# Optimization experiments

Measured on AMD Instinct MI355X. Metric: run time of the kernel, lower is better.

The kernel has to match this reference:

```python
import jax, jax.numpy as jnp
import numpy as np

HC = 4           # hc_mult
ITERS = 20       # hc_sinkhorn_iters
EPS = 1e-6       # hc_eps
NORM_EPS = 1e-6  # rms_norm_eps


def setup_inputs() -> dict:
    key = jax.random.key(0)
    k = jax.random.split(key, 4)
    B, S, H = 1, 4096, 4096
    mix = (2 + HC) * HC  # 24
    hidden_states = jax.random.normal(k[0], (B, S, HC, H), jnp.float32)
    hc_fn = jax.random.normal(k[1], (mix, HC * H), jnp.float32) * 0.02
    hc_base = jax.random.normal(k[2], (mix,), jnp.float32) * 0.02
    hc_scale = jnp.ones((3,), jnp.float32)
    norm_weight = jnp.ones((H,), jnp.float32)
    w_inner = jax.random.normal(k[3], (H, H), jnp.float32) * 0.02
    return {
        "hidden_states": hidden_states,
        "hc_fn": hc_fn,
        "hc_base": hc_base,
        "hc_scale": hc_scale,
        "norm_weight": norm_weight,
        "w_inner": w_inner,
    }


def reference(hidden_states, hc_fn, hc_base, hc_scale, norm_weight, w_inner):
    B, S, hc, H = hidden_states.shape
    # RMS stat over the flattened (hc*H) feature dim
    flat = hidden_states.reshape(B, S, hc * H).astype(jnp.float32)
    rs = jax.lax.rsqrt(jnp.mean(jnp.square(flat), axis=-1, keepdims=True) + NORM_EPS)
    mixes = jnp.einsum('bsd,md->bsm', flat, hc_fn) * rs  # [B,S,(2+hc)*hc]

    ps, qs, cs = hc_scale[0], hc_scale[1], hc_scale[2]
    pre = jax.nn.sigmoid(mixes[..., :hc] * ps + hc_base[:hc]) + EPS           # [B,S,hc]
    post = jax.nn.sigmoid(mixes[..., hc:2 * hc] * qs + hc_base[hc:2 * hc]) + EPS
    comb = jax.nn.sigmoid(
        mixes[..., 2 * hc:].reshape(B, S, hc, hc) * cs
        + hc_base[2 * hc:].reshape(hc, hc)
    ) + EPS  # [B,S,hc,hc]

    # 20-iter Sinkhorn row/column normalization
    def sink(_, c):
        c = c / (jnp.sum(c, axis=-1, keepdims=True) + EPS)
        return c / (jnp.sum(c, axis=-2, keepdims=True) + EPS)
    comb = jax.lax.fori_loop(0, ITERS, sink, comb)

    # weighted stream reduction -> [B,S,H]
    reduced = jnp.einsum('bsh,bshd->bsd', pre, hidden_states)

    # norm + inner sub-block (RMSNorm then dense projection)
    nr = jax.lax.rsqrt(jnp.mean(jnp.square(reduced), axis=-1, keepdims=True) + NORM_EPS)
    normed = reduced * nr * norm_weight
    out = jnp.einsum('bsd,ed->bse', normed, w_inner)  # [B,S,H]

    # broadcast back to streams: post-gated write + Sinkhorn-mixed residual
    expanded = post[..., None] * out[:, :, None, :] \
        + jnp.einsum('bshk,bskd->bshd', comb, hidden_states)
    return expanded.astype(hidden_states.dtype)
```

## Files before the change

### kernel.cpp

```cpp
#include <hip/hip_runtime.h>
#include <math.h>

#define S_DIM 4096
#define H_DIM 4096
#define HC_N 4
#define HD_DIM 16384
#define MIXN 24
#define SINK_IT 20
#define KSPL 32

typedef float f32x4 __attribute__((ext_vector_type(4)));
typedef __bf16 bf16x8 __attribute__((ext_vector_type(8)));
typedef unsigned short u16x8 __attribute__((ext_vector_type(8)));
typedef unsigned short u16x4 __attribute__((ext_vector_type(4)));

__device__ __forceinline__ unsigned short f2bf(float f) {
  unsigned u = __builtin_bit_cast(unsigned, f);
  u += 0x7FFFu + ((u >> 16) & 1u);
  return (unsigned short)(u >> 16);
}
__device__ __forceinline__ float bf2f(unsigned short h) {
  return __builtin_bit_cast(float, (unsigned)h << 16);
}

__global__ __launch_bounds__(256) void k_w2bf(const float* __restrict__ w,
                                              unsigned short* __restrict__ wb,
                                              const float* __restrict__ fn,
                                              unsigned short* __restrict__ fnb) {
  const int b = blockIdx.x;
  if (b < 8192) {
    const size_t i = (size_t)b * 2048 + threadIdx.x * 8;
    f32x4 a = *(const f32x4*)(w + i);
    f32x4 c = *(const f32x4*)(w + i + 4);
    u16x8 o;
    o[0] = f2bf(a.x); o[1] = f2bf(a.y); o[2] = f2bf(a.z); o[3] = f2bf(a.w);
    o[4] = f2bf(c.x); o[5] = f2bf(c.y); o[6] = f2bf(c.z); o[7] = f2bf(c.w);
    *(u16x8*)(wb + i) = o;
  } else if (b < 8384) {
    const size_t i = (size_t)(b - 8192) * 2048 + threadIdx.x * 8;
    f32x4 a = *(const f32x4*)(fn + i);
    f32x4 c = *(const f32x4*)(fn + i + 4);
    u16x8 o;
    o[0] = f2bf(a.x); o[1] = f2bf(a.y); o[2] = f2bf(a.z); o[3] = f2bf(a.w);
    o[4] = f2bf(c.x); o[5] = f2bf(c.y); o[6] = f2bf(c.z); o[7] = f2bf(c.w);
    *(u16x8*)(fnb + i) = o;
  } else {
    const size_t i = 393216 + (size_t)(b - 8384) * 2048 + threadIdx.x * 8;
    u16x8 o = {0, 0, 0, 0, 0, 0, 0, 0};
    *(u16x8*)(fnb + i) = o;
  }
}

__global__ __launch_bounds__(256) void k_mixgemm(const float* __restrict__ hs,
                                                 const unsigned short* __restrict__ fnb,
                                                 float* __restrict__ mixpart,
                                                 float* __restrict__ sumsqpart) {
  const int rt = blockIdx.x;
  const int p = blockIdx.y;
  const int tid = threadIdx.x, lane = tid & 63, wave = tid >> 6;
  const int r16 = lane & 15, kq = lane >> 4;
  const int row0 = rt * 128 + wave * 32;
  const size_t kbase = (size_t)p * 512 + kq * 8;

  f32x4 acc[2][2];
  f32x4 zero = {0.f, 0.f, 0.f, 0.f};
  acc[0][0] = zero; acc[0][1] = zero; acc[1][0] = zero; acc[1][1] = zero;
  float ss0 = 0.f, ss1 = 0.f;

  const float* a0 = hs + (size_t)(row0 + r16) * HD_DIM + kbase;
  const float* a1 = hs + (size_t)(row0 + 16 + r16) * HD_DIM + kbase;
  const unsigned short* b0p = fnb + (size_t)r16 * HD_DIM + kbase;
  const unsigned short* b1p = fnb + (size_t)(16 + r16) * HD_DIM + kbase;

#pragma unroll 4
  for (int kk = 0; kk < 512; kk += 32) {
    const f32x4 va0 = *(const f32x4*)(a0 + kk);
    const f32x4 va0b = *(const f32x4*)(a0 + kk + 4);
    const f32x4 va1 = *(const f32x4*)(a1 + kk);
    const f32x4 va1b = *(const f32x4*)(a1 + kk + 4);
    const bf16x8 fb0 = *(const bf16x8*)(b0p + kk);
    const bf16x8 fb1 = *(const bf16x8*)(b1p + kk);
    ss0 += va0.x * va0.x + va0.y * va0.y + va0.z * va0.z + va0.w * va0.w
         + va0b.x * va0b.x + va0b.y * va0b.y + va0b.z * va0b.z + va0b.w * va0b.w;
    ss1 += va1.x * va1.x + va1.y * va1.y + va1.z * va1.z + va1.w * va1.w
         + va1b.x * va1b.x + va1b.y * va1b.y + va1b.z * va1b.z + va1b.w * va1b.w;
    bf16x8 fa0, fa1;
    fa0[0] = (__bf16)va0.x; fa0[1] = (__bf16)va0.y; fa0[2] = (__bf16)va0.z; fa0[3] = (__bf16)va0.w;
    fa0[4] = (__bf16)va0b.x; fa0[5] = (__bf16)va0b.y; fa0[6] = (__bf16)va0b.z; fa0[7] = (__bf16)va0b.w;
    fa1[0] = (__bf16)va1.x; fa1[1] = (__bf16)va1.y; fa1[2] = (__bf16)va1.z; fa1[3] = (__bf16)va1.w;
    fa1[4] = (__bf16)va1b.x; fa1[5] = (__bf16)va1b.y; fa1[6] = (__bf16)va1b.z; fa1[7] = (__bf16)va1b.w;
    acc[0][0] = __builtin_amdgcn_mfma_f32_16x16x32_bf16(fa0, fb0, acc[0][0], 0, 0, 0);
    acc[0][1] = __builtin_amdgcn_mfma_f32_16x16x32_bf16(fa0, fb1, acc[0][1], 0, 0, 0);
    acc[1][0] = __builtin_amdgcn_mfma_f32_16x16x32_bf16(fa1, fb0, acc[1][0], 0, 0, 0);
    acc[1][1] = __builtin_amdgcn_mfma_f32_16x16x32_bf16(fa1, fb1, acc[1][1], 0, 0, 0);
  }

  ss0 += __shfl_xor(ss0, 16, 64); ss0 += __shfl_xor(ss0, 32, 64);
  ss1 += __shfl_xor(ss1, 16, 64); ss1 += __shfl_xor(ss1, 32, 64);
  if (lane < 16) {
    sumsqpart[(size_t)(row0 + lane) * KSPL + p] = ss0;
    sumsqpart[(size_t)(row0 + 16 + lane) * KSPL + p] = ss1;
  }

  const int cr = (lane >> 4) * 4, cc = lane & 15;
#pragma unroll
  for (int mi = 0; mi < 2; mi++)
#pragma unroll
    for (int ni = 0; ni < 2; ni++) {
      const int col = ni * 16 + cc;
      if (col < MIXN) {
#pragma unroll
        for (int j = 0; j < 4; j++) {
          const int row = row0 + mi * 16 + cr + j;
          mixpart[((size_t)row * KSPL + p) * MIXN + col] = acc[mi][ni][j];
        }
      }
    }
}

__global__ __launch_bounds__(256) void k_gates(const float* __restrict__ mixpart,
                                               const float* __restrict__ sumsqpart,
                                               const float* __restrict__ hbase,
                                               const float* __restrict__ hscale,
                                               float* __restrict__ gates) {
  const int row = blockIdx.x * 256 + threadIdx.x;
  float sumsq = 0.f;
  const float* sp = sumsqpart + (size_t)row * KSPL;
#pragma unroll
  for (int p = 0; p < KSPL; p++) sumsq += sp[p];
  float mr[MIXN];
#pragma unroll
  for (int m = 0; m < MIXN; m++) mr[m] = 0.f;
  const float* mp = mixpart + (size_t)row * KSPL * MIXN;
  for (int p = 0; p < KSPL; p++) {
#pragma unroll
    for (int m = 0; m < MIXN; m++) mr[m] += mp[p * MIXN + m];
  }
  const float rs = rsqrtf(sumsq * (1.0f / HD_DIM) + 1e-6f);
  const float ps = hscale[0], qs = hscale[1], cs = hscale[2];
  float g[MIXN];
#pragma unroll
  for (int m = 0; m < MIXN; m++) {
    const float sc = (m < 4) ? ps : ((m < 8) ? qs : cs);
    const float x = mr[m] * rs * sc + hbase[m];
    g[m] = 1.0f / (1.0f + expf(-x)) + 1e-6f;
  }
  for (int t = 0; t < SINK_IT; t++) {
#pragma unroll
    for (int i = 0; i < 4; i++) {
      const float s = g[8 + i * 4 + 0] + g[8 + i * 4 + 1] + g[8 + i * 4 + 2] + g[8 + i * 4 + 3] + 1e-6f;
#pragma unroll
      for (int j = 0; j < 4; j++) g[8 + i * 4 + j] /= s;
    }
#pragma unroll
    for (int j = 0; j < 4; j++) {
      const float s = g[8 + 0 + j] + g[8 + 4 + j] + g[8 + 8 + j] + g[8 + 12 + j] + 1e-6f;
#pragma unroll
      for (int i = 0; i < 4; i++) g[8 + i * 4 + j] /= s;
    }
  }
  float* go = gates + (size_t)row * MIXN;
#pragma unroll
  for (int m = 0; m < MIXN; m++) go[m] = g[m];
}

__global__ __launch_bounds__(256) void k_reduce_norm(const float* __restrict__ hs,
                                                     const float* __restrict__ gates,
                                                     const float* __restrict__ nw,
                                                     unsigned short* __restrict__ normed) {
  const int s = blockIdx.x, tid = threadIdx.x;
  const int lane = tid & 63, wave = tid >> 6;
  const float* g = gates + (size_t)s * MIXN;
  const float p0 = g[0], p1 = g[1], p2 = g[2], p3 = g[3];
  const size_t base = (size_t)s * HC_N * H_DIM;

  f32x4 red[4];
  float ssq = 0.f;
#pragma unroll
  for (int it = 0; it < 4; ++it) {
    const int d4 = it * 256 + tid;
    f32x4 a = *(const f32x4*)(hs + base + (size_t)0 * H_DIM + (size_t)d4 * 4);
    f32x4 b = *(const f32x4*)(hs + base + (size_t)1 * H_DIM + (size_t)d4 * 4);
    f32x4 c = *(const f32x4*)(hs + base + (size_t)2 * H_DIM + (size_t)d4 * 4);
    f32x4 d = *(const f32x4*)(hs + base + (size_t)3 * H_DIM + (size_t)d4 * 4);
    f32x4 v = p0 * a + p1 * b + p2 * c + p3 * d;
    red[it] = v;
    ssq += v.x * v.x + v.y * v.y + v.z * v.z + v.w * v.w;
  }
#pragma unroll
  for (int off = 32; off >= 1; off >>= 1) ssq += __shfl_xor(ssq, off, 64);
  __shared__ float ls[4];
  if (lane == 0) ls[wave] = ssq;
  __syncthreads();
  const float tot = ls[0] + ls[1] + ls[2] + ls[3];
  const float nr = rsqrtf(tot * (1.0f / H_DIM) + 1e-6f);
#pragma unroll
  for (int it = 0; it < 4; ++it) {
    const int d4 = it * 256 + tid;
    f32x4 w = *(const f32x4*)(nw + (size_t)d4 * 4);
    f32x4 v = red[it] * nr;
    v = v * w;
    u16x4 o;
    o[0] = f2bf(v.x); o[1] = f2bf(v.y); o[2] = f2bf(v.z); o[3] = f2bf(v.w);
    *(u16x4*)(normed + (size_t)s * H_DIM + (size_t)d4 * 4) = o;
  }
}

__device__ __forceinline__ void gload_lds16(const unsigned short* g, unsigned short* l) {
  __builtin_amdgcn_global_load_lds(
      (const __attribute__((address_space(1))) unsigned int*)(const void*)g,
      (__attribute__((address_space(3))) unsigned int*)(void*)l, 16, 0, 0);
}

__global__ __launch_bounds__(256, 4) void k_gemm(const unsigned short* __restrict__ A,
                                                 const unsigned short* __restrict__ B,
                                                 unsigned short* __restrict__ C) {
  __shared__ __align__(16) unsigned short sA[128 * 32];
  __shared__ __align__(16) unsigned short sB[128 * 32];
  const int tid = threadIdx.x;
  const int lane = tid & 63, wave = tid >> 6;
  const int bm = blockIdx.y, bn = blockIdx.x;
  const int wm = wave >> 1, wn = wave & 1;

  f32x4 zero = {0.f, 0.f, 0.f, 0.f};
  f32x4 acc[4][4];
#pragma unroll
  for (int mi = 0; mi < 4; mi++)
#pragma unroll
    for (int ni = 0; ni < 4; ni++) acc[mi][ni] = zero;

  const int strow = lane >> 2;
  const int stk = (((lane & 3) ^ ((lane >> 3) & 3)) * 8);
  const unsigned short* ga = A + (size_t)(bm * 128) * 4096;
  const unsigned short* gb = B + (size_t)(bn * 128) * 4096;
  const int c0 = wave * 2, c1 = wave * 2 + 1;

  const int rb = lane & 15;
  const int fk = (((lane >> 4) ^ ((lane >> 1) & 3)) * 8);

  for (int kk = 0; kk < 4096; kk += 32) {
    gload_lds16(ga + (size_t)(c0 * 16 + strow) * 4096 + kk + stk, sA + c0 * 512);
    gload_lds16(ga + (size_t)(c1 * 16 + strow) * 4096 + kk + stk, sA + c1 * 512);
    gload_lds16(gb + (size_t)(c0 * 16 + strow) * 4096 + kk + stk, sB + c0 * 512);
    gload_lds16(gb + (size_t)(c1 * 16 + strow) * 4096 + kk + stk, sB + c1 * 512);
    __syncthreads();

    bf16x8 af[4], bfr[4];
#pragma unroll
    for (int mi = 0; mi < 4; mi++)
      af[mi] = *(const bf16x8*)(sA + (wm * 64 + mi * 16 + rb) * 32 + fk);
#pragma unroll
    for (int ni = 0; ni < 4; ni++)
      bfr[ni] = *(const bf16x8*)(sB + (wn * 64 + ni * 16 + rb) * 32 + fk);
#pragma unroll
    for (int mi = 0; mi < 4; mi++)
#pragma unroll
      for (int ni = 0; ni < 4; ni++)
        acc[mi][ni] = __builtin_amdgcn_mfma_f32_16x16x32_bf16(af[mi], bfr[ni], acc[mi][ni], 0, 0, 0);
    __syncthreads();
  }

  const int cr = (lane >> 4) * 4, cc = lane & 15;
#pragma unroll
  for (int mi = 0; mi < 4; mi++)
#pragma unroll
    for (int ni = 0; ni < 4; ni++)
#pragma unroll
      for (int j = 0; j < 4; j++) {
        const int row = bm * 128 + wm * 64 + mi * 16 + cr + j;
        const int col = bn * 128 + wn * 64 + ni * 16 + cc;
        C[(size_t)row * 4096 + col] = f2bf(acc[mi][ni][j]);
      }
}

__global__ __launch_bounds__(256) void k_expand(const float* __restrict__ hs,
                                                const unsigned short* __restrict__ outb,
                                                const float* __restrict__ gates,
                                                float* __restrict__ y) {
  const int s = blockIdx.x, tid = threadIdx.x;
  const float* g = gates + (size_t)s * MIXN;
  float post[4], cb[4][4];
#pragma unroll
  for (int h = 0; h < 4; h++) post[h] = g[4 + h];
#pragma unroll
  for (int h = 0; h < 4; h++)
#pragma unroll
    for (int k = 0; k < 4; k++) cb[h][k] = g[8 + h * 4 + k];

  const size_t base = (size_t)s * HC_N * H_DIM;
#pragma unroll
  for (int it = 0; it < 4; ++it) {
    const int d4 = it * 256 + tid;
    f32x4 hv[4];
#pragma unroll
    for (int k = 0; k < 4; k++)
      hv[k] = *(const f32x4*)(hs + base + (size_t)k * H_DIM + (size_t)d4 * 4);
    u16x4 ob = *(const u16x4*)(outb + (size_t)s * H_DIM + (size_t)d4 * 4);
    f32x4 o = {bf2f(ob[0]), bf2f(ob[1]), bf2f(ob[2]), bf2f(ob[3])};
#pragma unroll
    for (int h = 0; h < 4; h++) {
      f32x4 e = post[h] * o + cb[h][0] * hv[0] + cb[h][1] * hv[1] + cb[h][2] * hv[2] + cb[h][3] * hv[3];
      *(f32x4*)(y + base + (size_t)h * H_DIM + (size_t)d4 * 4) = e;
    }
  }
}

extern "C" void kernel_launch(void* const* d_in, const int* in_sizes, int n_in,
                              void* d_out, int out_size, void* d_ws, size_t ws_size,
                              hipStream_t stream) {
  const float* hs = (const float*)d_in[0];
  const float* fn = (const float*)d_in[1];
  const float* hbase = (const float*)d_in[2];
  const float* hscale = (const float*)d_in[3];
  const float* nw = (const float*)d_in[4];
  const float* wi = (const float*)d_in[5];
  float* y = (float*)d_out;

  char* ws = (char*)d_ws;
  float* gates = (float*)(ws);
  float* sumsqpart = (float*)(ws + 524288);
  float* mixpart = (float*)(ws + 1048576);
  unsigned short* fnb = (unsigned short*)(ws + 13631488);
  unsigned short* normed = (unsigned short*)(ws + 16777216);
  unsigned short* wb = (unsigned short*)(ws + 50331648);
  unsigned short* outb = (unsigned short*)(ws + 83886080);

  k_w2bf<<<8448, 256, 0, stream>>>(wi, wb, fn, fnb);
  k_mixgemm<<<dim3(32, 32), 256, 0, stream>>>(hs, fnb, mixpart, sumsqpart);
  k_gates<<<16, 256, 0, stream>>>(mixpart, sumsqpart, hbase, hscale, gates);
  k_reduce_norm<<<4096, 256, 0, stream>>>(hs, gates, nw, normed);
  k_gemm<<<dim3(32, 32), 256, 0, stream>>>(normed, wb, outb);
  k_expand<<<4096, 256, 0, stream>>>(hs, outb, gates, y);
}
```

Baseline: 434.9 us.

## Emit bf16 hidden-state copy in mix GEMM and reuse it downstream

The mix GEMM already converts hidden_states to bf16, so it now also writes that bf16 copy to workspace. The reduce/norm and expand kernels then read this half-size copy instead of the fp32 tensor, cutting the bytes of the two later full passes. The split-K factor is doubled and the partial buffers are transposed. The gates kernel now spreads the partial-sum reduction across four wave groups through shared memory. The trade-off is an extra 128MB write, a large workspace requirement (with an fp32 fallback when it is too small), and a bf16-rounded residual term in the output.

After: 440.4 us. About the same (+1.3%).

```diff
diff --git a/kernel.cpp b/kernel.cpp
--- a/kernel.cpp
+++ b/kernel.cpp
@@ -7,7 +7,7 @@
 #define HD_DIM 16384
 #define MIXN 24
 #define SINK_IT 20
-#define KSPL 32
+#define KSPL 64
 
 typedef float f32x4 __attribute__((ext_vector_type(4)));
 typedef __bf16 bf16x8 __attribute__((ext_vector_type(8)));
@@ -51,16 +51,18 @@
   }
 }
 
+template<bool WH>
 __global__ __launch_bounds__(256) void k_mixgemm(const float* __restrict__ hs,
                                                  const unsigned short* __restrict__ fnb,
                                                  float* __restrict__ mixpart,
-                                                 float* __restrict__ sumsqpart) {
+                                                 float* __restrict__ sumsqpart,
+                                                 unsigned short* __restrict__ hsb) {
   const int rt = blockIdx.x;
   const int p = blockIdx.y;
   const int tid = threadIdx.x, lane = tid & 63, wave = tid >> 6;
   const int r16 = lane & 15, kq = lane >> 4;
   const int row0 = rt * 128 + wave * 32;
-  const size_t kbase = (size_t)p * 512 + kq * 8;
+  const size_t kbase = (size_t)p * 256 + kq * 8;
 
   f32x4 acc[2][2];
   f32x4 zero = {0.f, 0.f, 0.f, 0.f};
@@ -68,12 +70,13 @@
   float ss0 = 0.f, ss1 = 0.f;
 
   const float* a0 = hs + (size_t)(row0 + r16) * HD_DIM + kbase;
-  const float* a1 = hs + (size_t)(row0 + 16 + r16) * HD_DIM + kbase;
+  const float* a1 = a0 + (size_t)16 * HD_DIM;
   const unsigned short* b0p = fnb + (size_t)r16 * HD_DIM + kbase;
-  const unsigned short* b1p = fnb + (size_t)(16 + r16) * HD_DIM + kbase;
+  const unsigned short* b1p = b0p + (size_t)16 * HD_DIM;
+  unsigned short* h0 = hsb + (size_t)(row0 + r16) * HD_DIM + kbase;
 
 #pragma unroll 4
-  for (int kk = 0; kk < 512; kk += 32) {
+  for (int kk = 0; kk < 256; kk += 32) {
     const f32x4 va0 = *(const f32x4*)(a0 + kk);
     const f32x4 va0b = *(const f32x4*)(a0 + kk + 4);
     const f32x4 va1 = *(const f32x4*)(a1 + kk);
@@ -89,6 +92,10 @@
     fa0[4] = (__bf16)va0b.x; fa0[5] = (__bf16)va0b.y; fa0[6] = (__bf16)va0b.z; fa0[7] = (__bf16)va0b.w;
     fa1[0] = (__bf16)va1.x; fa1[1] = (__bf16)va1.y; fa1[2] = (__bf16)va1.z; fa1[3] = (__bf16)va1.w;
     fa1[4] = (__bf16)va1b.x; fa1[5] = (__bf16)va1b.y; fa1[6] = (__bf16)va1b.z; fa1[7] = (__bf16)va1b.w;
+    if (WH) {
+      *(bf16x8*)(h0 + kk) = fa0;
+      *(bf16x8*)(h0 + (size_t)16 * HD_DIM + kk) = fa1;
+    }
     acc[0][0] = __builtin_amdgcn_mfma_f32_16x16x32_bf16(fa0, fb0, acc[0][0], 0, 0, 0);
     acc[0][1] = __builtin_amdgcn_mfma_f32_16x16x32_bf16(fa0, fb1, acc[0][1], 0, 0, 0);
     acc[1][0] = __builtin_amdgcn_mfma_f32_16x16x32_bf16(fa1, fb0, acc[1][0], 0, 0, 0);
@@ -98,8 +105,8 @@
   ss0 += __shfl_xor(ss0, 16, 64); ss0 += __shfl_xor(ss0, 32, 64);
   ss1 += __shfl_xor(ss1, 16, 64); ss1 += __shfl_xor(ss1, 32, 64);
   if (lane < 16) {
-    sumsqpart[(size_t)(row0 + lane) * KSPL + p] = ss0;
-    sumsqpart[(size_t)(row0 + 16 + lane) * KSPL + p] = ss1;
+    sumsqpart[(size_t)p * S_DIM + row0 + lane] = ss0;
+    sumsqpart[(size_t)p * S_DIM + row0 + 16 + lane] = ss1;
   }
 
   const int cr = (lane >> 4) * 4, cc = lane & 15;
@@ -112,7 +119,7 @@
 #pragma unroll
         for (int j = 0; j < 4; j++) {
           const int row = row0 + mi * 16 + cr + j;
-          mixpart[((size_t)row * KSPL + p) * MIXN + col] = acc[mi][ni][j];
+          mixpart[((size_t)p * S_DIM + row) * MIXN + col] = acc[mi][ni][j];
         }
       }
     }
@@ -123,45 +130,54 @@
                                                const float* __restrict__ hbase,
                                                const float* __restrict__ hscale,
                                                float* __restrict__ gates) {
-  const int row = blockIdx.x * 256 + threadIdx.x;
-  float sumsq = 0.f;
-  const float* sp = sumsqpart + (size_t)row * KSPL;
-#pragma unroll
-  for (int p = 0; p < KSPL; p++) sumsq += sp[p];
+  __shared__ float sm[4][64][25];
+  const int t = threadIdx.x, rl = t & 63, pq = t >> 6;
+  const int row = blockIdx.x * 64 + rl;
   float mr[MIXN];
 #pragma unroll
   for (int m = 0; m < MIXN; m++) mr[m] = 0.f;
-  const float* mp = mixpart + (size_t)row * KSPL * MIXN;
-  for (int p = 0; p < KSPL; p++) {
-#pragma unroll
-    for (int m = 0; m < MIXN; m++) mr[m] += mp[p * MIXN + m];
-  }
-  const float rs = rsqrtf(sumsq * (1.0f / HD_DIM) + 1e-6f);
-  const float ps = hscale[0], qs = hscale[1], cs = hscale[2];
-  float g[MIXN];
-#pragma unroll
-  for (int m = 0; m < MIXN; m++) {
-    const float sc = (m < 4) ? ps : ((m < 8) ? qs : cs);
-    const float x = mr[m] * rs * sc + hbase[m];
-    g[m] = 1.0f / (1.0f + expf(-x)) + 1e-6f;
-  }
-  for (int t = 0; t < SINK_IT; t++) {
-#pragma unroll
-    for (int i = 0; i < 4; i++) {
-      const float s = g[8 + i * 4 + 0] + g[8 + i * 4 + 1] + g[8 + i * 4 + 2] + g[8 + i * 4 + 3] + 1e-6f;
-#pragma unroll
-      for (int j = 0; j < 4; j++) g[8 + i * 4 + j] /= s;
-    }
-#pragma unroll
-    for (int j = 0; j < 4; j++) {
-      const float s = g[8 + 0 + j] + g[8 + 4 + j] + g[8 + 8 + j] + g[8 + 12 + j] + 1e-6f;
-#pragma unroll
-      for (int i = 0; i < 4; i++) g[8 + i * 4 + j] /= s;
-    }
-  }
-  float* go = gates + (size_t)row * MIXN;
-#pragma unroll
-  for (int m = 0; m < MIXN; m++) go[m] = g[m];
+  float ss = 0.f;
+  for (int p = pq * 16; p < pq * 16 + 16; p++) {
+    const float* mp = mixpart + ((size_t)p * S_DIM + row) * MIXN;
+#pragma unroll
+    for (int m = 0; m < MIXN; m++) mr[m] += mp[m];
+    ss += sumsqpart[(size_t)p * S_DIM + row];
+  }
+#pragma unroll
+  for (int m = 0; m < MIXN; m++) sm[pq][rl][m] = mr[m];
+  sm[pq][rl][24] = ss;
+  __syncthreads();
+
+  if (t < 64) {
+    const int r2 = blockIdx.x * 64 + t;
+    float g[MIXN], sumsq = sm[0][t][24] + sm[1][t][24] + sm[2][t][24] + sm[3][t][24];
+    const float rs = rsqrtf(sumsq * (1.0f / HD_DIM) + 1e-6f);
+    const float ps = hscale[0], qs = hscale[1], cs = hscale[2];
+#pragma unroll
+    for (int m = 0; m < MIXN; m++) {
+      const float mv = sm[0][t][m] + sm[1][t][m] + sm[2][t][m] + sm[3][t][m];
+      const float sc = (m < 4) ? ps : ((m < 8) ? qs : cs);
+      const float x = mv * rs * sc + hbase[m];
+      g[m] = 1.0f / (1.0f + expf(-x)) + 1e-6f;
+    }
+    for (int it = 0; it < SINK_IT; it++) {
+#pragma unroll
+      for (int i = 0; i < 4; i++) {
+        const float s = g[8 + i * 4 + 0] + g[8 + i * 4 + 1] + g[8 + i * 4 + 2] + g[8 + i * 4 + 3] + 1e-6f;
+#pragma unroll
+        for (int j = 0; j < 4; j++) g[8 + i * 4 + j] /= s;
+      }
+#pragma unroll
+      for (int j = 0; j < 4; j++) {
+        const float s = g[8 + 0 + j] + g[8 + 4 + j] + g[8 + 8 + j] + g[8 + 12 + j] + 1e-6f;
+#pragma unroll
+        for (int i = 0; i < 4; i++) g[8 + i * 4 + j] /= s;
+      }
+    }
+    float* go = gates + (size_t)r2 * MIXN;
+#pragma unroll
+    for (int m = 0; m < MIXN; m++) go[m] = g[m];
+  }
 }
 
 __global__ __launch_bounds__(256) void k_reduce_norm(const float* __restrict__ hs,
@@ -206,6 +222,53 @@
   }
 }
 
+__global__ __launch_bounds__(256) void k_rn_bf(const unsigned short* __restrict__ hsb,
+                                               const float* __restrict__ gates,
+                                               const float* __restrict__ nw,
+                                               unsigned short* __restrict__ normed) {
+  const int s = blockIdx.x, tid = threadIdx.x;
+  const int lane = tid & 63, wave = tid >> 6;
+  const float* g = gates + (size_t)s * MIXN;
+  const float p0 = g[0], p1 = g[1], p2 = g[2], p3 = g[3];
+  const size_t base = (size_t)s * HC_N * H_DIM;
+
+  float red[16];
+  float ssq = 0.f;
+#pragma unroll
+  for (int it = 0; it < 2; ++it) {
+    const int d8 = (it * 256 + tid) * 8;
+    const u16x8 a = *(const u16x8*)(hsb + base + 0 * H_DIM + d8);
+    const u16x8 b = *(const u16x8*)(hsb + base + 1 * H_DIM + d8);
+    const u16x8 c = *(const u16x8*)(hsb + base + 2 * H_DIM + d8);
+    const u16x8 d = *(const u16x8*)(hsb + base + 3 * H_DIM + d8);
+#pragma unroll
+    for (int k = 0; k < 8; ++k) {
+      const float v = p0 * bf2f(a[k]) + p1 * bf2f(b[k]) + p2 * bf2f(c[k]) + p3 * bf2f(d[k]);
+      red[it * 8 + k] = v;
+      ssq += v * v;
+    }
+  }
+#pragma unroll
+  for (int off = 32; off >= 1; off >>= 1) ssq += __shfl_xor(ssq, off, 64);
+  __shared__ float ls[4];
+  if (lane == 0) ls[wave] = ssq;
+  __syncthreads();
+  const float tot = ls[0] + ls[1] + ls[2] + ls[3];
+  const float nr = rsqrtf(tot * (1.0f / H_DIM) + 1e-6f);
+#pragma unroll
+  for (int it = 0; it < 2; ++it) {
+    const int d8 = (it * 256 + tid) * 8;
+    const f32x4 w0 = *(const f32x4*)(nw + d8);
+    const f32x4 w1 = *(const f32x4*)(nw + d8 + 4);
+    u16x8 o;
+    o[0] = f2bf(red[it * 8 + 0] * nr * w0.x); o[1] = f2bf(red[it * 8 + 1] * nr * w0.y);
+    o[2] = f2bf(red[it * 8 + 2] * nr * w0.z); o[3] = f2bf(red[it * 8 + 3] * nr * w0.w);
+    o[4] = f2bf(red[it * 8 + 4] * nr * w1.x); o[5] = f2bf(red[it * 8 + 5] * nr * w1.y);
+    o[6] = f2bf(red[it * 8 + 6] * nr * w1.z); o[7] = f2bf(red[it * 8 + 7] * nr * w1.w);
+    *(u16x8*)(normed + (size_t)s * H_DIM + d8) = o;
+  }
+}
+
 __device__ __forceinline__ void gload_lds16(const unsigned short* g, unsigned short* l) {
   __builtin_amdgcn_global_load_lds(
       (const __attribute__((address_space(1))) unsigned int*)(const void*)g,
@@ -301,6 +364,44 @@
     for (int h = 0; h < 4; h++) {
       f32x4 e = post[h] * o + cb[h][0] * hv[0] + cb[h][1] * hv[1] + cb[h][2] * hv[2] + cb[h][3] * hv[3];
       *(f32x4*)(y + base + (size_t)h * H_DIM + (size_t)d4 * 4) = e;
+    }
+  }
+}
+
+__global__ __launch_bounds__(256) void k_expand_bf(const unsigned short* __restrict__ hsb,
+                                                   const unsigned short* __restrict__ outb,
+                                                   const float* __restrict__ gates,
+                                                   float* __restrict__ y) {
+  const int s = blockIdx.x, tid = threadIdx.x;
+  const float* g = gates + (size_t)s * MIXN;
+  float post[4], cb[4][4];
+#pragma unroll
+  for (int h = 0; h < 4; h++) post[h] = g[4 + h];
+#pragma unroll
+  for (int h = 0; h < 4; h++)
+#pragma unroll
+    for (int k = 0; k < 4; k++) cb[h][k] = g[8 + h * 4 + k];
+
+  const size_t base = (size_t)s * HC_N * H_DIM;
+#pragma unroll
+  for (int it = 0; it < 2; ++it) {
+    const int d8 = (it * 256 + tid) * 8;
+    const u16x8 a = *(const u16x8*)(hsb + base + 0 * H_DIM + d8);
+    const u16x8 b = *(const u16x8*)(hsb + base + 1 * H_DIM + d8);
+    const u16x8 c = *(const u16x8*)(hsb + base + 2 * H_DIM + d8);
+    const u16x8 d = *(const u16x8*)(hsb + base + 3 * H_DIM + d8);
+    const u16x8 ob = *(const u16x8*)(outb + (size_t)s * H_DIM + d8);
+#pragma unroll
+    for (int h = 0; h < 4; h++) {
+      float e[8];
+#pragma unroll
+      for (int k = 0; k < 8; ++k)
+        e[k] = post[h] * bf2f(ob[k]) + cb[h][0] * bf2f(a[k]) + cb[h][1] * bf2f(b[k])
+             + cb[h][2] * bf2f(c[k]) + cb[h][3] * bf2f(d[k]);
+      f32x4 e0 = {e[0], e[1], e[2], e[3]};
+      f32x4 e1 = {e[4], e[5], e[6], e[7]};
+      *(f32x4*)(y + base + (size_t)h * H_DIM + d8) = e0;
+      *(f32x4*)(y + base + (size_t)h * H_DIM + d8 + 4) = e1;
     }
   }
 }
@@ -319,16 +420,27 @@
   char* ws = (char*)d_ws;
   float* gates = (float*)(ws);
   float* sumsqpart = (float*)(ws + 524288);
-  float* mixpart = (float*)(ws + 1048576);
-  unsigned short* fnb = (unsigned short*)(ws + 13631488);
-  unsigned short* normed = (unsigned short*)(ws + 16777216);
-  unsigned short* wb = (unsigned short*)(ws + 50331648);
-  unsigned short* outb = (unsigned short*)(ws + 83886080);
+  float* mixpart = (float*)(ws + 2097152);
+  unsigned short* fnb = (unsigned short*)(ws + 29360128);
+  unsigned short* normed = (unsigned short*)(ws + 2097152);
+  unsigned short* wb = (unsigned short*)(ws + 37748736);
+  unsigned short* outb = (unsigned short*)(ws + 71303168);
+  unsigned short* hsb = (unsigned short*)(ws + 104857600);
+  const bool big = ws_size >= (size_t)104857600 + 134217728;
 
   k_w2bf<<<8448, 256, 0, stream>>>(wi, wb, fn, fnb);
-  k_mixgemm<<<dim3(32, 32), 256, 0, stream>>>(hs, fnb, mixpart, sumsqpart);
-  k_gates<<<16, 256, 0, stream>>>(mixpart, sumsqpart, hbase, hscale, gates);
-  k_reduce_norm<<<4096, 256, 0, stream>>>(hs, gates, nw, normed);
+  if (big)
+    k_mixgemm<true><<<dim3(32, KSPL), 256, 0, stream>>>(hs, fnb, mixpart, sumsqpart, hsb);
+  else
+    k_mixgemm<false><<<dim3(32, KSPL), 256, 0, stream>>>(hs, fnb, mixpart, sumsqpart, hsb);
+  k_gates<<<64, 256, 0, stream>>>(mixpart, sumsqpart, hbase, hscale, gates);
+  if (big)
+    k_rn_bf<<<4096, 256, 0, stream>>>(hsb, gates, nw, normed);
+  else
+    k_reduce_norm<<<4096, 256, 0, stream>>>(hs, gates, nw, normed);
   k_gemm<<<dim3(32, 32), 256, 0, stream>>>(normed, wb, outb);
-  k_expand<<<4096, 256, 0, stream>>>(hs, outb, gates, y);
-}
+  if (big)
+    k_expand_bf<<<4096, 256, 0, stream>>>(hsb, outb, gates, y);
+  else
+    k_expand<<<4096, 256, 0, stream>>>(hs, outb, gates, y);
+}
```
